# Performance work log

Hardware: AMD Instinct MI355X
Metric: run time of the kernel (lower is better)

## Reference

```python
import jax, jax.numpy as jnp
import numpy as np

N_HEADS = 16
ROPE_THETA = 10000.0


def _rope_tables(seq_len, head_dim, dtype=jnp.float32):
    half = head_dim // 2
    inv_freq = 1.0 / (ROPE_THETA ** (jnp.arange(0, half, dtype=jnp.float32) / half))
    t = jnp.arange(seq_len, dtype=jnp.float32)
    freqs = jnp.outer(t, inv_freq)  # (S, half)
    return jnp.cos(freqs).astype(dtype), jnp.sin(freqs).astype(dtype)


def _apply_rope(x, cos, sin):
    # x: (B, H, S, hd); cos/sin: (S, hd//2)
    half = x.shape[-1] // 2
    x1, x2 = x[..., :half], x[..., half:]
    c = cos[None, None, :, :]
    s = sin[None, None, :, :]
    return jnp.concatenate([x1 * c - x2 * s, x1 * s + x2 * c], axis=-1)


def setup_inputs() -> dict:
    key = jax.random.key(0)
    k1, k2, k3 = jax.random.split(key, 3)
    B, S, D = 4, 2048, 2048
    hd = D // N_HEADS
    x = jax.random.normal(k1, (B, S, D), dtype=jnp.float32)
    cos, sin = _rope_tables(S, hd)
    w_qkv = jax.random.normal(k2, (D, 3 * D), dtype=jnp.float32) * (D ** -0.5)
    w_out = jax.random.normal(k3, (D, D), dtype=jnp.float32) * (D ** -0.5)
    return {"x": x, "cos": cos, "sin": sin, "w_qkv": w_qkv, "w_out": w_out}


def reference(x, cos, sin, w_qkv, w_out):
    B, S, D = x.shape
    H = N_HEADS
    hd = D // H
    qkv = x @ w_qkv  # (B, S, 3D)
    qkv = qkv.reshape(B, S, 3, H, hd).transpose(2, 0, 3, 1, 4)  # (3, B, H, S, hd)
    q, k, v = qkv[0], qkv[1], qkv[2]
    q = _apply_rope(q, cos, sin)
    k = _apply_rope(k, cos, sin)
    scale = 1.0 / jnp.sqrt(jnp.asarray(hd, dtype=x.dtype))
    scores = jnp.einsum('bhqd,bhkd->bhqk', q, k) * scale  # (B, H, S, S)
    causal = jnp.tril(jnp.ones((S, S), dtype=bool))
    scores = jnp.where(causal[None, None, :, :], scores, jnp.asarray(-1e30, dtype=scores.dtype))
    p = jax.nn.softmax(scores, axis=-1)
    out = jnp.einsum('bhqk,bhkd->bhqd', p, v)  # (B, H, S, hd)
    out = out.transpose(0, 2, 1, 3).reshape(B, S, D)
    return out @ w_out
```

## Files before the change

kernel.cpp:

```cpp
#include <hip/hip_runtime.h>
#include <hip/hip_bf16.h>
#include <stdint.h>

typedef __bf16  bf16x8  __attribute__((ext_vector_type(8)));
typedef float   floatx4 __attribute__((ext_vector_type(4)));

typedef __attribute__((address_space(1))) void gvoid_t;
typedef __attribute__((address_space(3))) void svoid_t;

__device__ __forceinline__ void gld16(ushort* lds, const ushort* g) {
  __builtin_amdgcn_global_load_lds((gvoid_t*)g, (svoid_t*)lds, 16, 0, 0);
}

__device__ __forceinline__ ushort f2bf(float f) {
  union { float f; unsigned u; } v; v.f = f;
  unsigned u = v.u;
  return (ushort)((u + 0x7fffu + ((u >> 16) & 1u)) >> 16);
}
__device__ __forceinline__ float bf2f(ushort h) {
  union { unsigned u; float f; } v; v.u = ((unsigned)h) << 16; return v.f;
}
__device__ __forceinline__ unsigned pk2bf(float a, float b) {
  __hip_bfloat162 h = __float22bfloat162_rn(make_float2(a, b));
  union { __hip_bfloat162 h; unsigned u; } v; v.h = h; return v.u;
}

__global__ __launch_bounds__(256) void cvt_f32_bf16(
    const float* __restrict__ in, ushort* __restrict__ out) {
  int i = blockIdx.x * 256 + threadIdx.x;
  float4 a = ((const float4*)in)[i];
  ushort4 o;
  o.x = f2bf(a.x); o.y = f2bf(a.y); o.z = f2bf(a.z); o.w = f2bf(a.w);
  ((ushort4*)out)[i] = o;
}

__global__ __launch_bounds__(256) void transpose_cvt(
    const float* __restrict__ in, ushort* __restrict__ out, int R, int C) {
  __shared__ ushort tile[64][65];
  const int r0 = blockIdx.y * 64, c0 = blockIdx.x * 64;
  const int t = threadIdx.x;
#pragma unroll
  for (int rep = 0; rep < 16; rep++) {
    int idx = rep * 256 + t;
    int r = idx >> 6, c = idx & 63;
    tile[r][c] = f2bf(in[(size_t)(r0 + r) * C + c0 + c]);
  }
  __syncthreads();
#pragma unroll
  for (int rep = 0; rep < 16; rep++) {
    int idx = rep * 256 + t;
    int r = idx >> 6, c = idx & 63;
    out[(size_t)(c0 + r) * R + r0 + c] = tile[c][r];
  }
}

template <int EPI>
__global__ __launch_bounds__(512, 2) void gemm256(
    const ushort* __restrict__ A, const ushort* __restrict__ Bt,
    float* __restrict__ Cf,
    ushort* __restrict__ C0, ushort* __restrict__ C1, ushort* __restrict__ C2,
    int M, int N, int K) {
  __shared__ __align__(16) ushort As[2][256 * 64];
  __shared__ __align__(16) ushort Bs[2][256 * 64];
  const int t = threadIdx.x;
  const int lane = t & 63;
  const int w = t >> 6;
  const int l15 = lane & 15;
  const int quad = lane >> 4;
  const int m0 = blockIdx.y * 256;
  const int n0 = blockIdx.x * 256;
  const int wmB = (w >> 2) * 128;
  const int wnB = (w & 3) * 64;

  const int srow = t >> 3;
  const int sc = (t & 7) ^ (srow & 7);
  const ushort* pA = A + (size_t)(m0 + srow) * K + sc * 8;
  const ushort* pB = Bt + (size_t)(n0 + srow) * K + sc * 8;
  const size_t rstep = (size_t)64 * K;

  floatx4 acc[8][4];
  const floatx4 zero = {0.f, 0.f, 0.f, 0.f};
#pragma unroll
  for (int i = 0; i < 8; i++)
#pragma unroll
    for (int j = 0; j < 4; j++) acc[i][j] = zero;

  const int NT = K >> 6;

#pragma unroll
  for (int it = 0; it < 4; ++it)
    gld16(&As[0][(it * 512 + w * 64) * 8], pA + it * rstep);
#pragma unroll
  for (int it = 0; it < 4; ++it)
    gld16(&Bs[0][(it * 512 + w * 64) * 8], pB + it * rstep);

  for (int kt = 0; kt < NT; ++kt) {
    const int cb = kt & 1;
    const ushort* cA = As[cb];
    const ushort* cB = Bs[cb];
    ushort* nA = As[cb ^ 1];
    ushort* nB = Bs[cb ^ 1];
    const int kb2 = (kt + 1) << 6;
    const bool pf = (kt + 1 < NT);

    if (pf) {
      gld16(&nA[(0 * 512 + w * 64) * 8], pA + 0 * rstep + kb2);
      gld16(&nA[(1 * 512 + w * 64) * 8], pA + 1 * rstep + kb2);
      asm volatile("s_waitcnt vmcnt(2)" ::: "memory");
    } else {
      asm volatile("s_waitcnt vmcnt(0)" ::: "memory");
    }
    __builtin_amdgcn_s_barrier();

    bf16x8 bf[4];
#pragma unroll
    for (int kk = 0; kk < 2; ++kk) {
#pragma unroll
      for (int mh = 0; mh < 2; ++mh) {
        bf16x8 af[4];
#pragma unroll
        for (int m = 0; m < 4; ++m) {
          int row = wmB + (mh * 4 + m) * 16 + l15;
          int c = (kk * 4 + quad) ^ (row & 7);
          af[m] = *(const bf16x8*)&cA[row * 64 + c * 8];
        }
        if (mh == 0) {
#pragma unroll
          for (int n = 0; n < 4; ++n) {
            int row = wnB + n * 16 + l15;
            int c = (kk * 4 + quad) ^ (row & 7);
            bf[n] = *(const bf16x8*)&cB[row * 64 + c * 8];
          }
        }
        if (pf) {
          const int p = kk * 2 + mh;
          if (p == 0) {
            gld16(&nA[(2 * 512 + w * 64) * 8], pA + 2 * rstep + kb2);
            gld16(&nA[(3 * 512 + w * 64) * 8], pA + 3 * rstep + kb2);
          } else if (p == 1) {
            gld16(&nB[(0 * 512 + w * 64) * 8], pB + 0 * rstep + kb2);
            gld16(&nB[(1 * 512 + w * 64) * 8], pB + 1 * rstep + kb2);
          } else if (p == 2) {
            gld16(&nB[(2 * 512 + w * 64) * 8], pB + 2 * rstep + kb2);
            gld16(&nB[(3 * 512 + w * 64) * 8], pB + 3 * rstep + kb2);
          }
        }
        __builtin_amdgcn_s_barrier();
        asm volatile("s_waitcnt lgkmcnt(0)" ::: "memory");
        __builtin_amdgcn_sched_barrier(0);
        __builtin_amdgcn_s_setprio(1);
#pragma unroll
        for (int m = 0; m < 4; ++m)
#pragma unroll
          for (int n = 0; n < 4; ++n)
            acc[mh * 4 + m][n] = __builtin_amdgcn_mfma_f32_16x16x32_bf16(
                af[m], bf[n], acc[mh * 4 + m][n], 0, 0, 0);
        __builtin_amdgcn_s_setprio(0);
        __builtin_amdgcn_sched_barrier(0);
        __builtin_amdgcn_s_barrier();
      }
    }
  }

  if (EPI == 0) {
#pragma unroll
    for (int m = 0; m < 8; ++m)
#pragma unroll
      for (int n = 0; n < 4; ++n)
#pragma unroll
        for (int r = 0; r < 4; ++r) {
          int row = m0 + wmB + m * 16 + quad * 4 + r;
          int col = n0 + wnB + n * 16 + l15;
          Cf[(size_t)row * N + col] = acc[m][n][r];
        }
  } else {
    const int colW = n0 + wnB;
    const int sel = colW >> 11;
    const int h = (colW >> 7) & 15;
    if (sel < 2) {
      ushort* dst = (sel == 0) ? C0 : C1;
#pragma unroll
      for (int m = 0; m < 8; ++m) {
        int rowb = m0 + wmB + m * 16 + quad * 4;
        int b = rowb >> 11, s = rowb & 2047;
#pragma unroll
        for (int n = 0; n < 4; ++n) {
          int d = (colW + n * 16 + l15) & 127;
#pragma unroll
          for (int r = 0; r < 4; ++r)
            dst[((size_t)(b * 16 + h) * 2048 + (s + r)) * 128 + d] =
                f2bf(acc[m][n][r]);
        }
      }
    } else {
#pragma unroll
      for (int m = 0; m < 8; ++m) {
        int rowb = m0 + wmB + m * 16 + quad * 4;
        int b = rowb >> 11, s = rowb & 2047;
#pragma unroll
        for (int n = 0; n < 4; ++n) {
          int d = (colW + n * 16 + l15) & 127;
          ushort4 pk;
          pk.x = f2bf(acc[m][n][0]);
          pk.y = f2bf(acc[m][n][1]);
          pk.z = f2bf(acc[m][n][2]);
          pk.w = f2bf(acc[m][n][3]);
          *(ushort4*)&C2[((size_t)(b * 16 + h) * 128 + d) * 2048 + s] = pk;
        }
      }
    }
  }
}

__global__ __launch_bounds__(256) void rope_kernel(
    ushort* __restrict__ Q, ushort* __restrict__ Kb,
    const float* __restrict__ cosT, const float* __restrict__ sinT) {
  unsigned gid = blockIdx.x * 256u + threadIdx.x;
  int d = gid & 63;
  int s = (gid >> 6) & 2047;
  int bh = (gid >> 17) & 63;
  const bool isK = (gid >> 23) != 0;
  ushort* buf = isK ? Kb : Q;
  const float sc = isK ? 1.0f
                       : 0.08838834764831845f * 1.4426950408889634f;
  size_t base = ((size_t)bh * 2048 + s) * 128;
  float x1 = bf2f(buf[base + d]);
  float x2 = bf2f(buf[base + d + 64]);
  float c = cosT[s * 64 + d];
  float sn = sinT[s * 64 + d];
  buf[base + d] = f2bf((x1 * c - x2 * sn) * sc);
  buf[base + d + 64] = f2bf((x1 * sn + x2 * c) * sc);
}

__global__ __launch_bounds__(256, 4) void attn_kernel(
    const ushort* __restrict__ Q, const ushort* __restrict__ Kb,
    const ushort* __restrict__ VT, ushort* __restrict__ O) {
  __shared__ __align__(16) ushort Ks[64 * 128];
  __shared__ __align__(16) ushort Vs[128 * 64];
  __shared__ __align__(16) ushort Ps[64 * 64];
  const int t = threadIdx.x, lane = t & 63, w = t >> 6;
  const int l15 = lane & 15, quad = lane >> 4;
  const int bid = blockIdx.x;
  const int tq = 31 - (bid >> 6);
  const int bh = bid & 63;
  const int q0 = tq * 64 + w * 16;
  const int qrow = q0 + l15;
  const size_t hbase = (size_t)bh * 2048 * 128;
  const float NEGINF = -__builtin_inff();

  bf16x8 aq[4];
#pragma unroll
  for (int kb = 0; kb < 4; kb++)
    aq[kb] = *(const bf16x8*)&Q[hbase + (size_t)qrow * 128 + kb * 32 + quad * 8];

  float m2 = NEGINF, lsum = 0.f;
  floatx4 oacc[8];
  const floatx4 zero = {0.f, 0.f, 0.f, 0.f};
#pragma unroll
  for (int dj = 0; dj < 8; dj++) oacc[dj] = zero;

  const int ntk = tq + 1;

  for (int tk = 0; tk < ntk; tk++) {
    __syncthreads();
#pragma unroll
    for (int it = 0; it < 4; it++) {
      int o = (w * 4 + it) * 64 + lane;
      {
        int row = o >> 4;
        int c = (o & 15) ^ (row & 15);
        gld16(&Ks[(w * 4 + it) * 512],
              Kb + hbase + (size_t)(tk * 64 + row) * 128 + c * 8);
      }
      {
        int row = o >> 3;
        int c = (o & 7) ^ (row & 7);
        gld16(&Vs[(w * 4 + it) * 512],
              VT + hbase + (size_t)row * 2048 + tk * 64 + c * 8);
      }
    }
    __syncthreads();

    floatx4 sacc[4];
#pragma unroll
    for (int j = 0; j < 4; j++) sacc[j] = zero;
#pragma unroll
    for (int kb = 0; kb < 4; kb++) {
#pragma unroll
      for (int j = 0; j < 4; j++) {
        int row = j * 16 + l15;
        int c = (kb * 4 + quad) ^ (row & 15);
        bf16x8 kf = *(const bf16x8*)&Ks[row * 128 + c * 8];
        sacc[j] = __builtin_amdgcn_mfma_f32_16x16x32_bf16(kf, aq[kb], sacc[j],
                                                          0, 0, 0);
      }
    }

    if (tk == tq) {
#pragma unroll
      for (int j = 0; j < 4; j++)
#pragma unroll
        for (int r = 0; r < 4; r++) {
          int kcol = tk * 64 + j * 16 + quad * 4 + r;
          if (kcol > qrow) sacc[j][r] = NEGINF;
        }
    }

    float mx = sacc[0][0];
#pragma unroll
    for (int j = 0; j < 4; j++)
#pragma unroll
      for (int r = 0; r < 4; r++) mx = fmaxf(mx, sacc[j][r]);
    mx = fmaxf(mx, __shfl_xor(mx, 16));
    mx = fmaxf(mx, __shfl_xor(mx, 32));
    float mnew = fmaxf(m2, mx);
    float alpha = __builtin_exp2f(m2 - mnew);
    m2 = mnew;
    float rs = 0.f;
#pragma unroll
    for (int j = 0; j < 4; j++)
#pragma unroll
      for (int r = 0; r < 4; r++) {
        float p = __builtin_exp2f(sacc[j][r] - mnew);
        sacc[j][r] = p;
        rs += p;
      }
    rs += __shfl_xor(rs, 16);
    rs += __shfl_xor(rs, 32);
    lsum = lsum * alpha + rs;
    if (__any(alpha < 1.0f)) {
#pragma unroll
      for (int dj = 0; dj < 8; dj++) oacc[dj] *= alpha;
    }

#pragma unroll
    for (int j = 0; j < 4; j++) {
      unsigned lo = pk2bf(sacc[j][0], sacc[j][1]);
      unsigned hi = pk2bf(sacc[j][2], sacc[j][3]);
      int g = j * 2 + (quad >> 1);
      int gp = g ^ (l15 & 7);
      uint2 pv; pv.x = lo; pv.y = hi;
      *(uint2*)&Ps[(w * 16 + l15) * 64 + gp * 8 + (quad & 1) * 4] = pv;
    }

    bf16x8 bp[2];
#pragma unroll
    for (int kk = 0; kk < 2; kk++) {
      int g = kk * 4 + quad;
      int gp = g ^ (l15 & 7);
      bp[kk] = *(const bf16x8*)&Ps[(w * 16 + l15) * 64 + gp * 8];
    }
#pragma unroll
    for (int kk = 0; kk < 2; kk++)
#pragma unroll
      for (int dj = 0; dj < 8; dj++) {
        int rowd = dj * 16 + l15;
        int c = (kk * 4 + quad) ^ (rowd & 7);
        bf16x8 av = *(const bf16x8*)&Vs[rowd * 64 + c * 8];
        oacc[dj] = __builtin_amdgcn_mfma_f32_16x16x32_bf16(av, bp[kk], oacc[dj],
                                                           0, 0, 0);
      }
  }

  const int b = bh >> 4, h = bh & 15;
  const float rl = 1.0f / lsum;
  const size_t obase = ((size_t)(b * 2048 + qrow)) * 2048 + h * 128;
#pragma unroll
  for (int dj = 0; dj < 8; dj++) {
    ushort4 pk;
    pk.x = f2bf(oacc[dj][0] * rl);
    pk.y = f2bf(oacc[dj][1] * rl);
    pk.z = f2bf(oacc[dj][2] * rl);
    pk.w = f2bf(oacc[dj][3] * rl);
    *(ushort4*)&O[obase + dj * 16 + quad * 4] = pk;
  }
}

extern "C" void kernel_launch(void* const* d_in, const int* in_sizes, int n_in,
                              void* d_out, int out_size, void* d_ws, size_t ws_size,
                              hipStream_t stream) {
  const float* x    = (const float*)d_in[0];
  const float* cosT = (const float*)d_in[1];
  const float* sinT = (const float*)d_in[2];
  const float* wqkv = (const float*)d_in[3];
  const float* wout = (const float*)d_in[4];
  float* out = (float*)d_out;
  char* ws = (char*)d_ws;

  ushort* xbf   = (ushort*)d_out;
  ushort* wqkvT = (ushort*)(ws);
  ushort* Ob    = (ushort*)(ws);
  ushort* woutT = (ushort*)(ws + 33554432);
  ushort* Qb    = (ushort*)(ws + 41943040);
  ushort* Kbuf  = (ushort*)(ws + 75497472);
  ushort* VTb   = (ushort*)(ws + 109051904);

  cvt_f32_bf16<<<16384, 256, 0, stream>>>(x, xbf);
  transpose_cvt<<<dim3(96, 32), 256, 0, stream>>>(wqkv, wqkvT, 2048, 6144);
  transpose_cvt<<<dim3(32, 32), 256, 0, stream>>>(wout, woutT, 2048, 2048);
  gemm256<1><<<dim3(24, 32), 512, 0, stream>>>(xbf, wqkvT, nullptr,
                                               Qb, Kbuf, VTb, 8192, 6144, 2048);
  rope_kernel<<<65536, 256, 0, stream>>>(Qb, Kbuf, cosT, sinT);
  attn_kernel<<<2048, 256, 0, stream>>>(Qb, Kbuf, VTb, Ob);
  gemm256<0><<<dim3(8, 32), 512, 0, stream>>>(Ob, woutT, out,
                                              nullptr, nullptr, nullptr,
                                              8192, 2048, 2048);
}
```

Baseline: 606.7 us.

## Split GEMM LDS tiles into K-halves for deeper fine-grained prefetch pipeline

Restructures the 256x256 GEMM main loop so each 64-wide K tile is stored as two 32-wide halves, with loads issued per half-tile across eight phases per two K tiles. This keeps about three half-tiles in flight (vmcnt(8)) instead of one full tile, so global-to-LDS latency is hidden more deeply behind MFMA work. It uses a new XOR swizzle suited to 32-column rows and a hand-unrolled loop with a special tail. The LDS footprint is unchanged, but the code is more complex and relies on K being a multiple of 128.

```diff
diff --git a/kernel.cpp b/kernel.cpp
--- a/kernel.cpp
+++ b/kernel.cpp
@@ -60,8 +60,8 @@
     float* __restrict__ Cf,
     ushort* __restrict__ C0, ushort* __restrict__ C1, ushort* __restrict__ C2,
     int M, int N, int K) {
-  __shared__ __align__(16) ushort As[2][256 * 64];
-  __shared__ __align__(16) ushort Bs[2][256 * 64];
+  __shared__ __align__(16) ushort As[2][2][256 * 32];
+  __shared__ __align__(16) ushort Bs[2][2][256 * 32];
   const int t = threadIdx.x;
   const int lane = t & 63;
   const int w = t >> 6;
@@ -72,11 +72,22 @@
   const int wmB = (w >> 2) * 128;
   const int wnB = (w & 3) * 64;
 
-  const int srow = t >> 3;
-  const int sc = (t & 7) ^ (srow & 7);
-  const ushort* pA = A + (size_t)(m0 + srow) * K + sc * 8;
-  const ushort* pB = Bt + (size_t)(n0 + srow) * K + sc * 8;
-  const size_t rstep = (size_t)64 * K;
+  const int cS = (lane & 3) ^ ((lane >> 3) & 3);
+  const size_t aoff = (size_t)(m0 + w * 32 + (lane >> 2)) * K + cS * 8;
+  const size_t boff = (size_t)(n0 + w * 32 + (lane >> 2)) * K + cS * 8;
+
+#define STAGE_A(db, kh, tile)                                                \
+  { size_t ko_ = (size_t)(tile) * 64 + (kh) * 32;                            \
+    gld16(&As[db][kh][w * 1024],       A + aoff + ko_);                      \
+    gld16(&As[db][kh][w * 1024 + 512], A + aoff + 16 * (size_t)K + ko_); }
+#define STAGE_B(db, kh, tile)                                                \
+  { size_t ko_ = (size_t)(tile) * 64 + (kh) * 32;                            \
+    gld16(&Bs[db][kh][w * 1024],       Bt + boff + ko_);                     \
+    gld16(&Bs[db][kh][w * 1024 + 512], Bt + boff + 16 * (size_t)K + ko_); }
+
+#define W8 asm volatile("s_waitcnt vmcnt(8)" ::: "memory");
+#define W4 asm volatile("s_waitcnt vmcnt(4)" ::: "memory");
+#define W0 asm volatile("s_waitcnt vmcnt(0)" ::: "memory");
 
   floatx4 acc[8][4];
   const floatx4 zero = {0.f, 0.f, 0.f, 0.f};
@@ -85,82 +96,82 @@
 #pragma unroll
     for (int j = 0; j < 4; j++) acc[i][j] = zero;
 
-  const int NT = K >> 6;
-
-#pragma unroll
-  for (int it = 0; it < 4; ++it)
-    gld16(&As[0][(it * 512 + w * 64) * 8], pA + it * rstep);
-#pragma unroll
-  for (int it = 0; it < 4; ++it)
-    gld16(&Bs[0][(it * 512 + w * 64) * 8], pB + it * rstep);
-
-  for (int kt = 0; kt < NT; ++kt) {
-    const int cb = kt & 1;
-    const ushort* cA = As[cb];
-    const ushort* cB = Bs[cb];
-    ushort* nA = As[cb ^ 1];
-    ushort* nB = Bs[cb ^ 1];
-    const int kb2 = (kt + 1) << 6;
-    const bool pf = (kt + 1 < NT);
-
-    if (pf) {
-      gld16(&nA[(0 * 512 + w * 64) * 8], pA + 0 * rstep + kb2);
-      gld16(&nA[(1 * 512 + w * 64) * 8], pA + 1 * rstep + kb2);
-      asm volatile("s_waitcnt vmcnt(2)" ::: "memory");
+  bf16x8 bfr[4];
+
+#define PH(db, kh, mh, LB, STAGE, WAIT)                                        \
+  {                                                                            \
+    bf16x8 af[4];                                                              \
+    {                                                                          \
+      const ushort* Ah = &As[db][kh][0];                                       \
+      _Pragma("unroll") for (int m_ = 0; m_ < 4; ++m_) {                       \
+        int r_ = wmB + ((mh) * 4 + m_) * 16 + l15;                             \
+        int c_ = quad ^ ((r_ >> 1) & 3);                                       \
+        af[m_] = *(const bf16x8*)&Ah[r_ * 32 + c_ * 8];                        \
+      }                                                                        \
+      if (LB) {                                                                \
+        const ushort* Bh = &Bs[db][kh][0];                                     \
+        _Pragma("unroll") for (int n_ = 0; n_ < 4; ++n_) {                     \
+          int r_ = wnB + n_ * 16 + l15;                                        \
+          int c_ = quad ^ ((r_ >> 1) & 3);                                     \
+          bfr[n_] = *(const bf16x8*)&Bh[r_ * 32 + c_ * 8];                     \
+        }                                                                      \
+      }                                                                        \
+    }                                                                          \
+    STAGE                                                                      \
+    __builtin_amdgcn_s_barrier();                                              \
+    asm volatile("s_waitcnt lgkmcnt(0)" ::: "memory");                         \
+    __builtin_amdgcn_sched_barrier(0);                                         \
+    __builtin_amdgcn_s_setprio(1);                                             \
+    _Pragma("unroll") for (int m_ = 0; m_ < 4; ++m_)                           \
+      _Pragma("unroll") for (int n_ = 0; n_ < 4; ++n_)                         \
+        acc[(mh) * 4 + m_][n_] = __builtin_amdgcn_mfma_f32_16x16x32_bf16(      \
+            af[m_], bfr[n_], acc[(mh) * 4 + m_][n_], 0, 0, 0);                 \
+    __builtin_amdgcn_s_setprio(0);                                             \
+    __builtin_amdgcn_sched_barrier(0);                                         \
+    WAIT                                                                       \
+    __builtin_amdgcn_s_barrier();                                              \
+  }
+
+  const int NI = K >> 7;
+
+  STAGE_A(0, 0, 0);
+  STAGE_B(0, 0, 0);
+  STAGE_A(0, 1, 0);
+  STAGE_B(0, 1, 0);
+  STAGE_A(1, 0, 1);
+  STAGE_B(1, 0, 1);
+  W8
+  __builtin_amdgcn_s_barrier();
+
+  for (int i = 0; i < NI; ++i) {
+    const int t1 = 2 * i + 1, t2 = 2 * i + 2, t3 = 2 * i + 3;
+    if (i < NI - 1) {
+      PH(0, 0, 0, 1, STAGE_A(1, 1, t1), )
+      PH(0, 0, 1, 0, STAGE_B(1, 1, t1), W8)
+      PH(0, 1, 0, 1, STAGE_A(0, 0, t2), )
+      PH(0, 1, 1, 0, STAGE_B(0, 0, t2), W8)
+      PH(1, 0, 0, 1, STAGE_A(0, 1, t2), )
+      PH(1, 0, 1, 0, STAGE_B(0, 1, t2), W8)
+      PH(1, 1, 0, 1, STAGE_A(1, 0, t3), )
+      PH(1, 1, 1, 0, STAGE_B(1, 0, t3), W8)
     } else {
-      asm volatile("s_waitcnt vmcnt(0)" ::: "memory");
-    }
-    __builtin_amdgcn_s_barrier();
-
-    bf16x8 bf[4];
-#pragma unroll
-    for (int kk = 0; kk < 2; ++kk) {
-#pragma unroll
-      for (int mh = 0; mh < 2; ++mh) {
-        bf16x8 af[4];
-#pragma unroll
-        for (int m = 0; m < 4; ++m) {
-          int row = wmB + (mh * 4 + m) * 16 + l15;
-          int c = (kk * 4 + quad) ^ (row & 7);
-          af[m] = *(const bf16x8*)&cA[row * 64 + c * 8];
-        }
-        if (mh == 0) {
-#pragma unroll
-          for (int n = 0; n < 4; ++n) {
-            int row = wnB + n * 16 + l15;
-            int c = (kk * 4 + quad) ^ (row & 7);
-            bf[n] = *(const bf16x8*)&cB[row * 64 + c * 8];
-          }
-        }
-        if (pf) {
-          const int p = kk * 2 + mh;
-          if (p == 0) {
-            gld16(&nA[(2 * 512 + w * 64) * 8], pA + 2 * rstep + kb2);
-            gld16(&nA[(3 * 512 + w * 64) * 8], pA + 3 * rstep + kb2);
-          } else if (p == 1) {
-            gld16(&nB[(0 * 512 + w * 64) * 8], pB + 0 * rstep + kb2);
-            gld16(&nB[(1 * 512 + w * 64) * 8], pB + 1 * rstep + kb2);
-          } else if (p == 2) {
-            gld16(&nB[(2 * 512 + w * 64) * 8], pB + 2 * rstep + kb2);
-            gld16(&nB[(3 * 512 + w * 64) * 8], pB + 3 * rstep + kb2);
-          }
-        }
-        __builtin_amdgcn_s_barrier();
-        asm volatile("s_waitcnt lgkmcnt(0)" ::: "memory");
-        __builtin_amdgcn_sched_barrier(0);
-        __builtin_amdgcn_s_setprio(1);
-#pragma unroll
-        for (int m = 0; m < 4; ++m)
-#pragma unroll
-          for (int n = 0; n < 4; ++n)
-            acc[mh * 4 + m][n] = __builtin_amdgcn_mfma_f32_16x16x32_bf16(
-                af[m], bf[n], acc[mh * 4 + m][n], 0, 0, 0);
-        __builtin_amdgcn_s_setprio(0);
-        __builtin_amdgcn_sched_barrier(0);
-        __builtin_amdgcn_s_barrier();
-      }
-    }
-  }
+      PH(0, 0, 0, 1, STAGE_A(1, 1, t1), )
+      PH(0, 0, 1, 0, STAGE_B(1, 1, t1), W8)
+      PH(0, 1, 0, 1, , )
+      PH(0, 1, 1, 0, , W4)
+      PH(1, 0, 0, 1, , )
+      PH(1, 0, 1, 0, , W0)
+      PH(1, 1, 0, 1, , )
+      PH(1, 1, 1, 0, , )
+    }
+  }
+
+#undef PH
+#undef STAGE_A
+#undef STAGE_B
+#undef W8
+#undef W4
+#undef W0
 
   if (EPI == 0) {
 #pragma unroll
```

Measured after the change: 897.4 us. 47.9% more time.
